# Optimization experiments

Measured on AMD Instinct MI355X. Metric: run time of the kernel, lower is better.

The kernel has to match this reference:

```python
import jax, jax.numpy as jnp
import numpy as np

B, S, D = 4, 4096, 1024
EPS_LN = 1e-5
EPS_REC = 1e-8


def _layernorm(x, g, b):
    mu = jnp.mean(x, axis=-1, keepdims=True)
    var = jnp.mean((x - mu) ** 2, axis=-1, keepdims=True)
    return (x - mu) * jax.lax.rsqrt(var + EPS_LN) * g + b


def setup_inputs() -> dict:
    key = jax.random.key(0)
    ks = jax.random.split(key, 8)
    scale = 1.0 / np.sqrt(D)
    return {
        "x": jax.random.normal(ks[0], (B, S, D), dtype=jnp.float32),
        "x_prev": jax.random.normal(ks[1], (B, S, D), dtype=jnp.float32),
        "mu": jnp.float32(0.5),
        "decay_w": jax.random.uniform(ks[2], (D, 1), jnp.float32, -scale, scale),
        "decay_b": jnp.zeros((1,), jnp.float32),
        "ln1_g": jnp.ones((D,), jnp.float32),
        "ln1_b": jnp.zeros((D,), jnp.float32),
        "Wr_w": jax.random.uniform(ks[3], (D, D), jnp.float32, -scale, scale),
        "Wr_b": jnp.zeros((D,), jnp.float32),
        "Wv_w": jax.random.uniform(ks[4], (D, D), jnp.float32, -scale, scale),
        "Wv_b": jnp.zeros((D,), jnp.float32),
        "ln2_g": jnp.ones((D,), jnp.float32),
        "ln2_b": jnp.zeros((D,), jnp.float32),
    }


def reference(x, x_prev, mu, decay_w, decay_b, ln1_g, ln1_b,
              Wr_w, Wr_b, Wv_w, Wv_b, ln2_g, ln2_b):
    # Shift (token-mix by scalar mu)
    shifted = mu * x + (1.0 - mu) * x_prev  # [B,S,D]

    # SequenceMergingSeq with C = V = W = shifted
    decay = jax.nn.sigmoid(jnp.einsum("bsd,do->bso", shifted, decay_w) + decay_b)  # [B,S,1]
    e = jnp.exp(shifted)                       # [B,S,D]
    ea = jnp.sum(e, axis=-1, keepdims=True)    # [B,S,1]
    ev = e * shifted                           # [B,S,D]

    def step(carry, inp):
        a, b = carry
        d_t, ea_t, ev_t = inp
        a = d_t * a + ea_t            # [B,1]
        b = d_t * b + ev_t            # [B,D]
        return (a, b), b / (a + EPS_REC)

    init = (jnp.zeros((B, 1), shifted.dtype), jnp.zeros((B, D), shifted.dtype))
    xs = (jnp.swapaxes(decay, 0, 1), jnp.swapaxes(ea, 0, 1), jnp.swapaxes(ev, 0, 1))
    _, out_sbd = jax.lax.scan(step, init, xs)  # [S,B,D]
    merged = _layernorm(jnp.swapaxes(out_sbd, 0, 1), ln1_g, ln1_b)  # [B,S,D]

    # StateCoupling
    gate = jax.nn.sigmoid(jnp.einsum("bsd,ed->bse", merged, Wr_w) + Wr_b)
    value = jnp.einsum("bsd,ed->bse", merged, Wv_w) + Wv_b
    coupled = _layernorm(gate * value, ln2_g, ln2_b)

    return shifted + coupled
```

## Files before the change

### kernel.cpp

```cpp
#include <hip/hip_runtime.h>

#define BATCH 4
#define SEQ   4096
#define DIM   1024
#define NCH   512
#define CHK   8
#define NROWS (BATCH*SEQ)

typedef __attribute__((ext_vector_type(4))) float f32x4;
typedef __attribute__((ext_vector_type(8))) short shortx8;
typedef __attribute__((ext_vector_type(4))) short shortx4;

static __device__ __forceinline__ unsigned short f2bf(float f){
    unsigned int u = __float_as_uint(f);
    u += 0x7FFFu + ((u >> 16) & 1u);
    return (unsigned short)(u >> 16);
}
static __device__ __forceinline__ float bf2f(unsigned short h){
    return __uint_as_float(((unsigned int)h) << 16);
}
static __device__ __forceinline__ float sigmoidf_fast(float x){
    return 1.0f / (1.0f + __expf(-x));
}
static __device__ __forceinline__ shortx4 pack4(f32x4 s){
    shortx4 o;
    o.x = (short)f2bf(s.x); o.y = (short)f2bf(s.y);
    o.z = (short)f2bf(s.z); o.w = (short)f2bf(s.w);
    return o;
}

__global__ __launch_bounds__(256) void k_pack_w(
    const float* __restrict__ Wr, const float* __restrict__ Wv,
    unsigned short* __restrict__ Wcat)
{
    const int n = blockIdx.x;
    const int grp = n >> 5, r = n & 31;
    const float* src = (r < 16) ? (Wr + (size_t)(grp*16 + r)*DIM)
                                : (Wv + (size_t)(grp*16 + (r-16))*DIM);
    const int tid = threadIdx.x;
    f32x4 v = reinterpret_cast<const f32x4*>(src)[tid];
    reinterpret_cast<shortx4*>(Wcat)[n*256 + tid] = pack4(v);
}

__global__ __launch_bounds__(256) void k_shift_scan(
    const float* __restrict__ X, const float* __restrict__ XP,
    const float* __restrict__ mu_p, const float* __restrict__ dw,
    const float* __restrict__ db_p,
    unsigned short* __restrict__ shifted,
    float* __restrict__ b_local, float* __restrict__ a_local,
    float* __restrict__ cumP)
{
    const int tid  = threadIdx.x;
    const int lane = tid & 63;
    const int wid  = tid >> 6;
    const int cid  = blockIdx.x*4 + wid;
    const int batch = cid >> 9;
    const int chunk = cid & (NCH-1);
    const int row0  = batch*SEQ + chunk*CHK;

    const float mu = mu_p[0];
    const float om = 1.0f - mu;
    const float db = db_p[0];

    const f32x4* dwv = reinterpret_cast<const f32x4*>(dw);
    const f32x4 w0 = dwv[lane], w1 = dwv[64+lane], w2 = dwv[128+lane], w3 = dwv[192+lane];

    f32x4 b0 = {0,0,0,0}, b1 = {0,0,0,0}, b2 = {0,0,0,0}, b3 = {0,0,0,0};
    float a_run = 0.f, cp = 1.f;

    const f32x4* Xv  = reinterpret_cast<const f32x4*>(X);
    const f32x4* XPv = reinterpret_cast<const f32x4*>(XP);
    f32x4*  BL = reinterpret_cast<f32x4*>(b_local);
    shortx4* SH = reinterpret_cast<shortx4*>(shifted);

    for (int r = 0; r < CHK; ++r){
        const int row = row0 + r;
        const int rb  = row*(DIM/4);

        f32x4 x0 = Xv[rb+lane],     x1 = Xv[rb+64+lane],
              x2 = Xv[rb+128+lane], x3 = Xv[rb+192+lane];
        f32x4 p0 = XPv[rb+lane],     p1 = XPv[rb+64+lane],
              p2 = XPv[rb+128+lane], p3 = XPv[rb+192+lane];
        f32x4 s0 = mu*x0 + om*p0, s1 = mu*x1 + om*p1;
        f32x4 s2 = mu*x2 + om*p2, s3 = mu*x3 + om*p3;

        SH[rb+lane]     = pack4(s0);
        SH[rb+64+lane]  = pack4(s1);
        SH[rb+128+lane] = pack4(s2);
        SH[rb+192+lane] = pack4(s3);

        float dot = s0.x*w0.x + s0.y*w0.y + s0.z*w0.z + s0.w*w0.w
                  + s1.x*w1.x + s1.y*w1.y + s1.z*w1.z + s1.w*w1.w
                  + s2.x*w2.x + s2.y*w2.y + s2.z*w2.z + s2.w*w2.w
                  + s3.x*w3.x + s3.y*w3.y + s3.z*w3.z + s3.w*w3.w;

        f32x4 e0, e1, e2, e3;
        e0.x=__expf(s0.x); e0.y=__expf(s0.y); e0.z=__expf(s0.z); e0.w=__expf(s0.w);
        e1.x=__expf(s1.x); e1.y=__expf(s1.y); e1.z=__expf(s1.z); e1.w=__expf(s1.w);
        e2.x=__expf(s2.x); e2.y=__expf(s2.y); e2.z=__expf(s2.z); e2.w=__expf(s2.w);
        e3.x=__expf(s3.x); e3.y=__expf(s3.y); e3.z=__expf(s3.z); e3.w=__expf(s3.w);
        float ea = e0.x+e0.y+e0.z+e0.w + e1.x+e1.y+e1.z+e1.w
                 + e2.x+e2.y+e2.z+e2.w + e3.x+e3.y+e3.z+e3.w;

        #pragma unroll
        for (int off = 1; off < 64; off <<= 1){
            dot += __shfl_xor(dot, off, 64);
            ea  += __shfl_xor(ea,  off, 64);
        }

        const float dt = sigmoidf_fast(dot + db);
        a_run = dt*a_run + ea;
        cp   *= dt;
        b0 = dt*b0 + e0*s0;  b1 = dt*b1 + e1*s1;
        b2 = dt*b2 + e2*s2;  b3 = dt*b3 + e3*s3;

        BL[rb+lane]     = b0;
        BL[rb+64+lane]  = b1;
        BL[rb+128+lane] = b2;
        BL[rb+192+lane] = b3;
        if (lane == 0){ a_local[row] = a_run; cumP[row] = cp; }
    }
}

__global__ __launch_bounds__(256) void k_combine(
    const float* __restrict__ b_local, const float* __restrict__ a_local,
    const float* __restrict__ cumP,
    float* __restrict__ carryA, float* __restrict__ carryB)
{
    const int batch = blockIdx.x >> 2;
    const int dseg  = blockIdx.x & 3;
    const int d = dseg*256 + threadIdx.x;

    __shared__ float sP[NCH], sA[NCH];
    for (int c = threadIdx.x; c < NCH; c += 256){
        const int er = batch*SEQ + c*CHK + (CHK-1);
        sP[c] = cumP[er];
        sA[c] = a_local[er];
    }
    __syncthreads();

    const float* bl = b_local + (size_t)batch*SEQ*DIM;
    float* cB = carryB + (size_t)batch*NCH*DIM;
    const bool wA = (dseg == 0 && threadIdx.x == 0);

    float cb = 0.f, ca = 0.f;
    float f0 = bl[(0*CHK+CHK-1)*DIM + d];
    float f1 = bl[(1*CHK+CHK-1)*DIM + d];
    float f2 = bl[(2*CHK+CHK-1)*DIM + d];
    float f3 = bl[(3*CHK+CHK-1)*DIM + d];

    for (int c = 0; c < NCH; c += 4){
        const float v0=f0, v1=f1, v2=f2, v3=f3;
        if (c+4 < NCH){
            f0 = bl[((c+4)*CHK+CHK-1)*DIM + d];
            f1 = bl[((c+5)*CHK+CHK-1)*DIM + d];
            f2 = bl[((c+6)*CHK+CHK-1)*DIM + d];
            f3 = bl[((c+7)*CHK+CHK-1)*DIM + d];
        }
        cB[(c+0)*DIM + d] = cb; if (wA) carryA[batch*NCH + c+0] = ca;
        cb = sP[c+0]*cb + v0;   ca = sP[c+0]*ca + sA[c+0];
        cB[(c+1)*DIM + d] = cb; if (wA) carryA[batch*NCH + c+1] = ca;
        cb = sP[c+1]*cb + v1;   ca = sP[c+1]*ca + sA[c+1];
        cB[(c+2)*DIM + d] = cb; if (wA) carryA[batch*NCH + c+2] = ca;
        cb = sP[c+2]*cb + v2;   ca = sP[c+2]*ca + sA[c+2];
        cB[(c+3)*DIM + d] = cb; if (wA) carryA[batch*NCH + c+3] = ca;
        cb = sP[c+3]*cb + v3;   ca = sP[c+3]*ca + sA[c+3];
    }
}

static __device__ __forceinline__ void block_reduce2(float& s, float& s2, float* red, int tid){
    #pragma unroll
    for (int off = 1; off < 64; off <<= 1){
        s  += __shfl_xor(s,  off, 64);
        s2 += __shfl_xor(s2, off, 64);
    }
    const int wid = tid >> 6, lane = tid & 63;
    if (lane == 0){ red[wid] = s; red[4+wid] = s2; }
    __syncthreads();
    s  = red[0]+red[1]+red[2]+red[3];
    s2 = red[4]+red[5]+red[6]+red[7];
}

__global__ __launch_bounds__(256) void k_fix_ln1(
    const float* __restrict__ b_local, const float* __restrict__ a_local,
    const float* __restrict__ cumP, const float* __restrict__ carryA,
    const float* __restrict__ carryB,
    const float* __restrict__ g1, const float* __restrict__ bb1,
    unsigned short* __restrict__ merged)
{
    const int row = blockIdx.x;
    const int batch = row >> 12;
    const int t = row & (SEQ-1);
    const int c = t >> 3;
    const int tid = threadIdx.x;

    const float cpv = cumP[row];
    const float a = a_local[row] + cpv * carryA[batch*NCH + c];
    const float inv_a = 1.0f / (a + 1e-8f);

    f32x4 bl = reinterpret_cast<const f32x4*>(b_local)[row*256 + tid];
    f32x4 cb = reinterpret_cast<const f32x4*>(carryB)[(batch*NCH + c)*256 + tid];
    f32x4 o = (bl + cpv*cb) * inv_a;

    float s  = o.x+o.y+o.z+o.w;
    float s2 = o.x*o.x + o.y*o.y + o.z*o.z + o.w*o.w;
    __shared__ float red[8];
    block_reduce2(s, s2, red, tid);

    const float mean = s * (1.0f/DIM);
    const float rstd = rsqrtf(s2*(1.0f/DIM) - mean*mean + 1e-5f);
    f32x4 gg = reinterpret_cast<const f32x4*>(g1)[tid];
    f32x4 bb = reinterpret_cast<const f32x4*>(bb1)[tid];
    f32x4 m = (o - mean)*rstd*gg + bb;
    reinterpret_cast<shortx4*>(merged)[row*256 + tid] = pack4(m);
}

typedef __attribute__((address_space(3))) unsigned int lds_uint;
typedef __attribute__((address_space(1))) unsigned int glob_uint;
static __device__ __forceinline__ void stage16(const unsigned short* g, unsigned short* l){
    __builtin_amdgcn_global_load_lds((const glob_uint*)g, (lds_uint*)l, 16, 0, 0);
}

__global__ __launch_bounds__(256) void k_gemm(
    const unsigned short* __restrict__ A,
    const unsigned short* __restrict__ Bt,
    const float* __restrict__ rbias, const float* __restrict__ vbias,
    float* __restrict__ gv)
{
    __shared__ __align__(16) unsigned short As[128*32];
    __shared__ __align__(16) unsigned short Bs[128*32];
    const int tid  = threadIdx.x;
    const int lane = tid & 63;
    const int wid  = tid >> 6;
    const int nt = blockIdx.x & 15;
    const int mt = blockIdx.x >> 4;
    const int m0 = mt*128, n0 = nt*128;
    const int wr = wid >> 1, wc = wid & 1;

    f32x4 acc[4][4];
    #pragma unroll
    for (int i = 0; i < 4; ++i)
        #pragma unroll
        for (int j = 0; j < 4; ++j) acc[i][j] = (f32x4){0.f,0.f,0.f,0.f};

    const int srow = tid >> 2;
    const int scol = (tid & 3) << 3;
    const unsigned short* gA0 = A  + (size_t)(m0 + srow)*DIM + scol;
    const unsigned short* gA1 = A  + (size_t)(m0 + 64 + srow)*DIM + scol;
    const unsigned short* gB0 = Bt + (size_t)(n0 + srow)*DIM + scol;
    const unsigned short* gB1 = Bt + (size_t)(n0 + 64 + srow)*DIM + scol;
    unsigned short* lA0 = As + wid*512;
    unsigned short* lA1 = As + 2048 + wid*512;
    unsigned short* lB0 = Bs + wid*512;
    unsigned short* lB1 = Bs + 2048 + wid*512;

    const int fr = lane & 15, fq = lane >> 4;

    for (int kt = 0; kt < DIM/32; ++kt){
        __syncthreads();
        const int ko = kt*32;
        stage16(gA0 + ko, lA0);
        stage16(gA1 + ko, lA1);
        stage16(gB0 + ko, lB0);
        stage16(gB1 + ko, lB1);
        __syncthreads();

        shortx8 af[4], bfv[4];
        #pragma unroll
        for (int f = 0; f < 4; ++f){
            af[f]  = *reinterpret_cast<const shortx8*>(&As[(wr*64 + f*16 + fr)*32 + fq*8]);
            bfv[f] = *reinterpret_cast<const shortx8*>(&Bs[(wc*64 + f*16 + fr)*32 + fq*8]);
        }
        #pragma unroll
        for (int i = 0; i < 4; ++i)
            #pragma unroll
            for (int j = 0; j < 4; ++j)
                acc[i][j] = __builtin_amdgcn_mfma_f32_16x16x32_bf16(af[i], bfv[j], acc[i][j], 0, 0, 0);
    }

    #pragma unroll
    for (int p = 0; p < 2; ++p){
        const int e = (nt*4 + wc*2 + p)*16 + fr;
        const float rbe = rbias[e], vbe = vbias[e];
        #pragma unroll
        for (int i = 0; i < 4; ++i){
            f32x4 ga = acc[i][2*p], va = acc[i][2*p+1];
            const int mrow = m0 + wr*64 + i*16 + fq*4;
            #pragma unroll
            for (int q = 0; q < 4; ++q){
                const float gate = sigmoidf_fast(ga[q] + rbe);
                gv[(size_t)(mrow+q)*DIM + e] = gate * (va[q] + vbe);
            }
        }
    }
}

__global__ __launch_bounds__(256) void k_ln2_res(
    const float* __restrict__ gvb, const unsigned short* __restrict__ shifted,
    const float* __restrict__ g2, const float* __restrict__ b2,
    float* __restrict__ out)
{
    const int row = blockIdx.x, tid = threadIdx.x;
    const int idx = row*256 + tid;
    f32x4 v = reinterpret_cast<const f32x4*>(gvb)[idx];
    float s  = v.x+v.y+v.z+v.w;
    float s2 = v.x*v.x + v.y*v.y + v.z*v.z + v.w*v.w;
    __shared__ float red[8];
    block_reduce2(s, s2, red, tid);
    const float mean = s * (1.0f/DIM);
    const float rstd = rsqrtf(s2*(1.0f/DIM) - mean*mean + 1e-5f);
    f32x4 gg = reinterpret_cast<const f32x4*>(g2)[tid];
    f32x4 bb = reinterpret_cast<const f32x4*>(b2)[tid];
    f32x4 nv = (v - mean)*rstd*gg + bb;
    shortx4 sh = reinterpret_cast<const shortx4*>(shifted)[idx];
    f32x4 o;
    o.x = bf2f((unsigned short)sh.x) + nv.x;
    o.y = bf2f((unsigned short)sh.y) + nv.y;
    o.z = bf2f((unsigned short)sh.z) + nv.z;
    o.w = bf2f((unsigned short)sh.w) + nv.w;
    reinterpret_cast<f32x4*>(out)[idx] = o;
}

extern "C" void kernel_launch(void* const* d_in, const int* in_sizes, int n_in,
                              void* d_out, int out_size, void* d_ws, size_t ws_size,
                              hipStream_t stream)
{
    (void)in_sizes; (void)n_in; (void)out_size; (void)ws_size;
    const float* x     = (const float*)d_in[0];
    const float* xprev = (const float*)d_in[1];
    const float* mu    = (const float*)d_in[2];
    const float* dw    = (const float*)d_in[3];
    const float* db    = (const float*)d_in[4];
    const float* ln1g  = (const float*)d_in[5];
    const float* ln1b  = (const float*)d_in[6];
    const float* Wr    = (const float*)d_in[7];
    const float* Wrb   = (const float*)d_in[8];
    const float* Wv    = (const float*)d_in[9];
    const float* Wvb   = (const float*)d_in[10];
    const float* ln2g  = (const float*)d_in[11];
    const float* ln2b  = (const float*)d_in[12];
    float* out = (float*)d_out;

    char* ws = (char*)d_ws;
    size_t off = 0;
    auto alloc = [&](size_t bytes) -> void* {
        void* p = ws + off;
        off += (bytes + 255) & ~(size_t)255;
        return p;
    };
    unsigned short* shifted = (unsigned short*)alloc((size_t)NROWS*DIM*2);
    float* b_local          = (float*)alloc((size_t)NROWS*DIM*4);
    unsigned short* merged  = (unsigned short*)alloc((size_t)NROWS*DIM*2);
    float* carryB           = (float*)alloc((size_t)BATCH*NCH*DIM*4);
    unsigned short* Wcat    = (unsigned short*)alloc((size_t)2048*1024*2);
    float* a_local          = (float*)alloc((size_t)NROWS*4);
    float* cumP             = (float*)alloc((size_t)NROWS*4);
    float* carryA           = (float*)alloc((size_t)BATCH*NCH*4);
    float* gvbuf = b_local;

    hipLaunchKernelGGL(k_pack_w,    dim3(2048),  dim3(256),  0, stream, Wr, Wv, Wcat);
    hipLaunchKernelGGL(k_shift_scan,dim3(512),   dim3(256),  0, stream,
                       x, xprev, mu, dw, db, shifted, b_local, a_local, cumP);
    hipLaunchKernelGGL(k_combine,   dim3(16),    dim3(256),  0, stream,
                       b_local, a_local, cumP, carryA, carryB);
    hipLaunchKernelGGL(k_fix_ln1,   dim3(16384), dim3(256),  0, stream,
                       b_local, a_local, cumP, carryA, carryB, ln1g, ln1b, merged);
    hipLaunchKernelGGL(k_gemm,      dim3(2048),  dim3(256),  0, stream,
                       merged, Wcat, Wrb, Wvb, gvbuf);
    hipLaunchKernelGGL(k_ln2_res,   dim3(16384), dim3(256),  0, stream,
                       gvbuf, shifted, ln2g, ln2b, out);
}
```

Before: 237.1 us.

## Store scan intermediates in bf16 and pipeline a larger-tile MFMA GEMM

The scan partials (b_local), the chunk carries (carryB) and the gated GEMM output are now stored as bf16 instead of fp32, which halves the main intermediate memory traffic between kernels. The GEMM is rewritten to use 256x128 tiles, 512 threads and a K-step of 64. It triple-buffers LDS through async global-to-LDS loads with explicit waitcnt and barriers, adds a swizzled LDS layout and s_setprio around the MFMA bursts, and writes results out through an LDS-staged, coalesced epilogue. The cost is extra rounding error in the recurrence and the LayerNorm inputs, plus a large LDS footprint (144 KB per block) that limits occupancy.

```diff
diff --git a/kernel.cpp b/kernel.cpp
--- a/kernel.cpp
+++ b/kernel.cpp
@@ -6,6 +6,7 @@
 #define NCH   512
 #define CHK   8
 #define NROWS (BATCH*SEQ)
+#define NT    16
 
 typedef __attribute__((ext_vector_type(4))) float f32x4;
 typedef __attribute__((ext_vector_type(8))) short shortx8;
@@ -26,6 +27,12 @@
     shortx4 o;
     o.x = (short)f2bf(s.x); o.y = (short)f2bf(s.y);
     o.z = (short)f2bf(s.z); o.w = (short)f2bf(s.w);
+    return o;
+}
+static __device__ __forceinline__ f32x4 unpack4(shortx4 s){
+    f32x4 o;
+    o.x = bf2f((unsigned short)s.x); o.y = bf2f((unsigned short)s.y);
+    o.z = bf2f((unsigned short)s.z); o.w = bf2f((unsigned short)s.w);
     return o;
 }
 
@@ -47,7 +54,7 @@
     const float* __restrict__ mu_p, const float* __restrict__ dw,
     const float* __restrict__ db_p,
     unsigned short* __restrict__ shifted,
-    float* __restrict__ b_local, float* __restrict__ a_local,
+    unsigned short* __restrict__ b_local, float* __restrict__ a_local,
     float* __restrict__ cumP)
 {
     const int tid  = threadIdx.x;
@@ -70,7 +77,7 @@
 
     const f32x4* Xv  = reinterpret_cast<const f32x4*>(X);
     const f32x4* XPv = reinterpret_cast<const f32x4*>(XP);
-    f32x4*  BL = reinterpret_cast<f32x4*>(b_local);
+    shortx4* BL = reinterpret_cast<shortx4*>(b_local);
     shortx4* SH = reinterpret_cast<shortx4*>(shifted);
 
     for (int r = 0; r < CHK; ++r){
@@ -114,18 +121,18 @@
         b0 = dt*b0 + e0*s0;  b1 = dt*b1 + e1*s1;
         b2 = dt*b2 + e2*s2;  b3 = dt*b3 + e3*s3;
 
-        BL[rb+lane]     = b0;
-        BL[rb+64+lane]  = b1;
-        BL[rb+128+lane] = b2;
-        BL[rb+192+lane] = b3;
+        BL[rb+lane]     = pack4(b0);
+        BL[rb+64+lane]  = pack4(b1);
+        BL[rb+128+lane] = pack4(b2);
+        BL[rb+192+lane] = pack4(b3);
         if (lane == 0){ a_local[row] = a_run; cumP[row] = cp; }
     }
 }
 
 __global__ __launch_bounds__(256) void k_combine(
-    const float* __restrict__ b_local, const float* __restrict__ a_local,
+    const unsigned short* __restrict__ b_local, const float* __restrict__ a_local,
     const float* __restrict__ cumP,
-    float* __restrict__ carryA, float* __restrict__ carryB)
+    float* __restrict__ carryA, unsigned short* __restrict__ carryB)
 {
     const int batch = blockIdx.x >> 2;
     const int dseg  = blockIdx.x & 3;
@@ -139,31 +146,31 @@
     }
     __syncthreads();
 
-    const float* bl = b_local + (size_t)batch*SEQ*DIM;
-    float* cB = carryB + (size_t)batch*NCH*DIM;
+    const unsigned short* bl = b_local + (size_t)batch*SEQ*DIM;
+    unsigned short* cB = carryB + (size_t)batch*NCH*DIM;
     const bool wA = (dseg == 0 && threadIdx.x == 0);
 
     float cb = 0.f, ca = 0.f;
-    float f0 = bl[(0*CHK+CHK-1)*DIM + d];
-    float f1 = bl[(1*CHK+CHK-1)*DIM + d];
-    float f2 = bl[(2*CHK+CHK-1)*DIM + d];
-    float f3 = bl[(3*CHK+CHK-1)*DIM + d];
+    float f0 = bf2f(bl[(0*CHK+CHK-1)*DIM + d]);
+    float f1 = bf2f(bl[(1*CHK+CHK-1)*DIM + d]);
+    float f2 = bf2f(bl[(2*CHK+CHK-1)*DIM + d]);
+    float f3 = bf2f(bl[(3*CHK+CHK-1)*DIM + d]);
 
     for (int c = 0; c < NCH; c += 4){
         const float v0=f0, v1=f1, v2=f2, v3=f3;
         if (c+4 < NCH){
-            f0 = bl[((c+4)*CHK+CHK-1)*DIM + d];
-            f1 = bl[((c+5)*CHK+CHK-1)*DIM + d];
-            f2 = bl[((c+6)*CHK+CHK-1)*DIM + d];
-            f3 = bl[((c+7)*CHK+CHK-1)*DIM + d];
+            f0 = bf2f(bl[((c+4)*CHK+CHK-1)*DIM + d]);
+            f1 = bf2f(bl[((c+5)*CHK+CHK-1)*DIM + d]);
+            f2 = bf2f(bl[((c+6)*CHK+CHK-1)*DIM + d]);
+            f3 = bf2f(bl[((c+7)*CHK+CHK-1)*DIM + d]);
         }
-        cB[(c+0)*DIM + d] = cb; if (wA) carryA[batch*NCH + c+0] = ca;
+        cB[(c+0)*DIM + d] = f2bf(cb); if (wA) carryA[batch*NCH + c+0] = ca;
         cb = sP[c+0]*cb + v0;   ca = sP[c+0]*ca + sA[c+0];
-        cB[(c+1)*DIM + d] = cb; if (wA) carryA[batch*NCH + c+1] = ca;
+        cB[(c+1)*DIM + d] = f2bf(cb); if (wA) carryA[batch*NCH + c+1] = ca;
         cb = sP[c+1]*cb + v1;   ca = sP[c+1]*ca + sA[c+1];
-        cB[(c+2)*DIM + d] = cb; if (wA) carryA[batch*NCH + c+2] = ca;
+        cB[(c+2)*DIM + d] = f2bf(cb); if (wA) carryA[batch*NCH + c+2] = ca;
         cb = sP[c+2]*cb + v2;   ca = sP[c+2]*ca + sA[c+2];
-        cB[(c+3)*DIM + d] = cb; if (wA) carryA[batch*NCH + c+3] = ca;
+        cB[(c+3)*DIM + d] = f2bf(cb); if (wA) carryA[batch*NCH + c+3] = ca;
         cb = sP[c+3]*cb + v3;   ca = sP[c+3]*ca + sA[c+3];
     }
 }
@@ -182,9 +189,9 @@
 }
 
 __global__ __launch_bounds__(256) void k_fix_ln1(
-    const float* __restrict__ b_local, const float* __restrict__ a_local,
+    const unsigned short* __restrict__ b_local, const float* __restrict__ a_local,
     const float* __restrict__ cumP, const float* __restrict__ carryA,
-    const float* __restrict__ carryB,
+    const unsigned short* __restrict__ carryB,
     const float* __restrict__ g1, const float* __restrict__ bb1,
     unsigned short* __restrict__ merged)
 {
@@ -198,8 +205,8 @@
     const float a = a_local[row] + cpv * carryA[batch*NCH + c];
     const float inv_a = 1.0f / (a + 1e-8f);
 
-    f32x4 bl = reinterpret_cast<const f32x4*>(b_local)[row*256 + tid];
-    f32x4 cb = reinterpret_cast<const f32x4*>(carryB)[(batch*NCH + c)*256 + tid];
+    f32x4 bl = unpack4(reinterpret_cast<const shortx4*>(b_local)[row*256 + tid]);
+    f32x4 cb = unpack4(reinterpret_cast<const shortx4*>(carryB)[(batch*NCH + c)*256 + tid]);
     f32x4 o = (bl + cpv*cb) * inv_a;
 
     float s  = o.x+o.y+o.z+o.w;
@@ -217,92 +224,149 @@
 
 typedef __attribute__((address_space(3))) unsigned int lds_uint;
 typedef __attribute__((address_space(1))) unsigned int glob_uint;
-static __device__ __forceinline__ void stage16(const unsigned short* g, unsigned short* l){
+static __device__ __forceinline__ void gload16(const unsigned short* g, char* l){
     __builtin_amdgcn_global_load_lds((const glob_uint*)g, (lds_uint*)l, 16, 0, 0);
 }
-
-__global__ __launch_bounds__(256) void k_gemm(
+#define SBAR() do { __builtin_amdgcn_sched_barrier(0); __builtin_amdgcn_s_barrier(); __builtin_amdgcn_sched_barrier(0); } while(0)
+
+__global__ __launch_bounds__(512, 2) void k_gemm(
     const unsigned short* __restrict__ A,
     const unsigned short* __restrict__ Bt,
     const float* __restrict__ rbias, const float* __restrict__ vbias,
-    float* __restrict__ gv)
-{
-    __shared__ __align__(16) unsigned short As[128*32];
-    __shared__ __align__(16) unsigned short Bs[128*32];
+    unsigned short* __restrict__ gv)
+{
+    __shared__ __align__(16) char lds[3*49152];
     const int tid  = threadIdx.x;
     const int lane = tid & 63;
     const int wid  = tid >> 6;
-    const int nt = blockIdx.x & 15;
-    const int mt = blockIdx.x >> 4;
-    const int m0 = mt*128, n0 = nt*128;
-    const int wr = wid >> 1, wc = wid & 1;
-
-    f32x4 acc[4][4];
+    const int wm   = wid >> 2;
+    const int wn   = wid & 3;
+
+    const int bid  = blockIdx.x;
+    const int wgid = (bid & 7)*128 + (bid >> 3);
+    const int mt = wgid >> 4, nt = wgid & 15;
+    const int m0 = mt*256, n0 = nt*128;
+
+    const int sr  = lane >> 2;
+    const int scg = (lane & 3) ^ (((lane >> 5) & 1) << 1);
+    const unsigned short* gA = A  + (size_t)(m0 + wid*16 + sr)*DIM + scg*8;
+    const unsigned short* gB = Bt + (size_t)(n0 + wid*16 + sr)*DIM + scg*8;
+
+    const int fr = lane & 15, fq = lane >> 4;
+    const int soff = fr*64 + ((fq*16) ^ ((fr & 8) ? 32 : 0));
+
+    f32x4 acc[8][2];
     #pragma unroll
-    for (int i = 0; i < 4; ++i)
-        #pragma unroll
-        for (int j = 0; j < 4; ++j) acc[i][j] = (f32x4){0.f,0.f,0.f,0.f};
-
-    const int srow = tid >> 2;
-    const int scol = (tid & 3) << 3;
-    const unsigned short* gA0 = A  + (size_t)(m0 + srow)*DIM + scol;
-    const unsigned short* gA1 = A  + (size_t)(m0 + 64 + srow)*DIM + scol;
-    const unsigned short* gB0 = Bt + (size_t)(n0 + srow)*DIM + scol;
-    const unsigned short* gB1 = Bt + (size_t)(n0 + 64 + srow)*DIM + scol;
-    unsigned short* lA0 = As + wid*512;
-    unsigned short* lA1 = As + 2048 + wid*512;
-    unsigned short* lB0 = Bs + wid*512;
-    unsigned short* lB1 = Bs + 2048 + wid*512;
-
-    const int fr = lane & 15, fq = lane >> 4;
-
-    for (int kt = 0; kt < DIM/32; ++kt){
-        __syncthreads();
-        const int ko = kt*32;
-        stage16(gA0 + ko, lA0);
-        stage16(gA1 + ko, lA1);
-        stage16(gB0 + ko, lB0);
-        stage16(gB1 + ko, lB1);
-        __syncthreads();
-
-        shortx8 af[4], bfv[4];
-        #pragma unroll
-        for (int f = 0; f < 4; ++f){
-            af[f]  = *reinterpret_cast<const shortx8*>(&As[(wr*64 + f*16 + fr)*32 + fq*8]);
-            bfv[f] = *reinterpret_cast<const shortx8*>(&Bs[(wc*64 + f*16 + fr)*32 + fq*8]);
+    for (int i = 0; i < 8; ++i){ acc[i][0] = (f32x4){0,0,0,0}; acc[i][1] = (f32x4){0,0,0,0}; }
+
+    auto STAGE_A = [&](int buf, int tk){
+        char* dst = &lds[buf*49152 + wid*2048];
+        const unsigned short* src = gA + tk*64;
+        gload16(src,             dst);
+        gload16(src + 32,        dst + 1024);
+        gload16(src + 128*DIM,      dst + 16384);
+        gload16(src + 128*DIM + 32, dst + 16384 + 1024);
+    };
+    auto STAGE_B = [&](int buf, int tk){
+        char* dst = &lds[buf*49152 + 32768 + wid*2048];
+        const unsigned short* src = gB + tk*64;
+        gload16(src,      dst);
+        gload16(src + 32, dst + 1024);
+    };
+
+    STAGE_A(0, 0); STAGE_B(0, 0);
+    STAGE_A(1, 1); STAGE_B(1, 1);
+    asm volatile("s_waitcnt vmcnt(6)" ::: "memory");
+    SBAR();
+
+    int bc = 0, bn = 2;
+    for (int t = 0; t < NT; ++t){
+        const char* bufA = &lds[bc*49152];
+        const char* bufB = bufA + 32768;
+
+        shortx8 bq[2][2], af[4][2];
+        #pragma unroll
+        for (int nf = 0; nf < 2; ++nf)
+            #pragma unroll
+            for (int ks = 0; ks < 2; ++ks)
+                bq[nf][ks] = *reinterpret_cast<const shortx8*>(bufB + ((wn*2+nf)*2+ks)*1024 + soff);
+        #pragma unroll
+        for (int mf = 0; mf < 4; ++mf)
+            #pragma unroll
+            for (int ks = 0; ks < 2; ++ks)
+                af[mf][ks] = *reinterpret_cast<const shortx8*>(bufA + wm*16384 + (mf*2+ks)*1024 + soff);
+        if (t < NT-2) STAGE_A(bn, t+2);
+        SBAR();
+        __builtin_amdgcn_s_setprio(1);
+        #pragma unroll
+        for (int mf = 0; mf < 4; ++mf)
+            #pragma unroll
+            for (int nf = 0; nf < 2; ++nf){
+                acc[mf][nf] = __builtin_amdgcn_mfma_f32_16x16x32_bf16(af[mf][0], bq[nf][0], acc[mf][nf], 0,0,0);
+                acc[mf][nf] = __builtin_amdgcn_mfma_f32_16x16x32_bf16(af[mf][1], bq[nf][1], acc[mf][nf], 0,0,0);
+            }
+        __builtin_amdgcn_s_setprio(0);
+        SBAR();
+
+        #pragma unroll
+        for (int mf = 0; mf < 4; ++mf)
+            #pragma unroll
+            for (int ks = 0; ks < 2; ++ks)
+                af[mf][ks] = *reinterpret_cast<const shortx8*>(bufA + wm*16384 + ((mf+4)*2+ks)*1024 + soff);
+        if (t < NT-2){
+            STAGE_B(bn, t+2);
+            asm volatile("s_waitcnt vmcnt(6)" ::: "memory");
+        } else {
+            asm volatile("s_waitcnt vmcnt(0)" ::: "memory");
         }
-        #pragma unroll
-        for (int i = 0; i < 4; ++i)
+        SBAR();
+        __builtin_amdgcn_s_setprio(1);
+        #pragma unroll
+        for (int mf = 0; mf < 4; ++mf)
             #pragma unroll
-            for (int j = 0; j < 4; ++j)
-                acc[i][j] = __builtin_amdgcn_mfma_f32_16x16x32_bf16(af[i], bfv[j], acc[i][j], 0, 0, 0);
-    }
-
+            for (int nf = 0; nf < 2; ++nf){
+                acc[mf+4][nf] = __builtin_amdgcn_mfma_f32_16x16x32_bf16(af[mf][0], bq[nf][0], acc[mf+4][nf], 0,0,0);
+                acc[mf+4][nf] = __builtin_amdgcn_mfma_f32_16x16x32_bf16(af[mf][1], bq[nf][1], acc[mf+4][nf], 0,0,0);
+            }
+        __builtin_amdgcn_s_setprio(0);
+        SBAR();
+
+        bc = (bc == 2) ? 0 : bc+1;
+        bn = (bn == 2) ? 0 : bn+1;
+    }
+
+    __syncthreads();
+    unsigned short* ep = reinterpret_cast<unsigned short*>(lds);
+    const int e = (nt*4 + wn)*16 + fr;
+    const float rbe = rbias[e], vbe = vbias[e];
     #pragma unroll
-    for (int p = 0; p < 2; ++p){
-        const int e = (nt*4 + wc*2 + p)*16 + fr;
-        const float rbe = rbias[e], vbe = vbias[e];
-        #pragma unroll
-        for (int i = 0; i < 4; ++i){
-            f32x4 ga = acc[i][2*p], va = acc[i][2*p+1];
-            const int mrow = m0 + wr*64 + i*16 + fq*4;
-            #pragma unroll
-            for (int q = 0; q < 4; ++q){
-                const float gate = sigmoidf_fast(ga[q] + rbe);
-                gv[(size_t)(mrow+q)*DIM + e] = gate * (va[q] + vbe);
-            }
+    for (int mf = 0; mf < 8; ++mf){
+        const int rbase = wm*128 + mf*16 + fq*4;
+        #pragma unroll
+        for (int q = 0; q < 4; ++q){
+            const float g = sigmoidf_fast(acc[mf][0][q] + rbe);
+            const float v = acc[mf][1][q] + vbe;
+            ep[(rbase + q)*64 + wn*16 + fr] = f2bf(g*v);
         }
     }
+    __syncthreads();
+    #pragma unroll
+    for (int p = 0; p < 4; ++p){
+        const int row = p*64 + (tid >> 3);
+        const int cg8 = tid & 7;
+        shortx8 val = *reinterpret_cast<const shortx8*>(&ep[row*64 + cg8*8]);
+        *reinterpret_cast<shortx8*>(&gv[(size_t)(m0+row)*DIM + nt*64 + cg8*8]) = val;
+    }
 }
 
 __global__ __launch_bounds__(256) void k_ln2_res(
-    const float* __restrict__ gvb, const unsigned short* __restrict__ shifted,
+    const unsigned short* __restrict__ gvb, const unsigned short* __restrict__ shifted,
     const float* __restrict__ g2, const float* __restrict__ b2,
     float* __restrict__ out)
 {
     const int row = blockIdx.x, tid = threadIdx.x;
     const int idx = row*256 + tid;
-    f32x4 v = reinterpret_cast<const f32x4*>(gvb)[idx];
+    f32x4 v = unpack4(reinterpret_cast<const shortx4*>(gvb)[idx]);
     float s  = v.x+v.y+v.z+v.w;
     float s2 = v.x*v.x + v.y*v.y + v.z*v.z + v.w*v.w;
     __shared__ float red[8];
@@ -312,13 +376,8 @@
     f32x4 gg = reinterpret_cast<const f32x4*>(g2)[tid];
     f32x4 bb = reinterpret_cast<const f32x4*>(b2)[tid];
     f32x4 nv = (v - mean)*rstd*gg + bb;
-    shortx4 sh = reinterpret_cast<const shortx4*>(shifted)[idx];
-    f32x4 o;
-    o.x = bf2f((unsigned short)sh.x) + nv.x;
-    o.y = bf2f((unsigned short)sh.y) + nv.y;
-    o.z = bf2f((unsigned short)sh.z) + nv.z;
-    o.w = bf2f((unsigned short)sh.w) + nv.w;
-    reinterpret_cast<f32x4*>(out)[idx] = o;
+    f32x4 sh = unpack4(reinterpret_cast<const shortx4*>(shifted)[idx]);
+    reinterpret_cast<f32x4*>(out)[idx] = sh + nv;
 }
 
 extern "C" void kernel_launch(void* const* d_in, const int* in_sizes, int n_in,
@@ -349,24 +408,24 @@
         return p;
     };
     unsigned short* shifted = (unsigned short*)alloc((size_t)NROWS*DIM*2);
-    float* b_local          = (float*)alloc((size_t)NROWS*DIM*4);
+    unsigned short* b_local = (unsigned short*)alloc((size_t)NROWS*DIM*2);
     unsigned short* merged  = (unsigned short*)alloc((size_t)NROWS*DIM*2);
-    float* carryB           = (float*)alloc((size_t)BATCH*NCH*DIM*4);
+    unsigned short* carryB  = (unsigned short*)alloc((size_t)BATCH*NCH*DIM*2);
     unsigned short* Wcat    = (unsigned short*)alloc((size_t)2048*1024*2);
     float* a_local          = (float*)alloc((size_t)NROWS*4);
     float* cumP             = (float*)alloc((size_t)NROWS*4);
     float* carryA           = (float*)alloc((size_t)BATCH*NCH*4);
-    float* gvbuf = b_local;
-
-    hipLaunchKernelGGL(k_pack_w,    dim3(2048),  dim3(256),  0, stream, Wr, Wv, Wcat);
-    hipLaunchKernelGGL(k_shift_scan,dim3(512),   dim3(256),  0, stream,
+    unsigned short* gvbuf   = b_local;
+
+    hipLaunchKernelGGL(k_pack_w,    dim3(2048),  dim3(256), 0, stream, Wr, Wv, Wcat);
+    hipLaunchKernelGGL(k_shift_scan,dim3(512),   dim3(256), 0, stream,
                        x, xprev, mu, dw, db, shifted, b_local, a_local, cumP);
-    hipLaunchKernelGGL(k_combine,   dim3(16),    dim3(256),  0, stream,
+    hipLaunchKernelGGL(k_combine,   dim3(16),    dim3(256), 0, stream,
                        b_local, a_local, cumP, carryA, carryB);
-    hipLaunchKernelGGL(k_fix_ln1,   dim3(16384), dim3(256),  0, stream,
+    hipLaunchKernelGGL(k_fix_ln1,   dim3(16384), dim3(256), 0, stream,
                        b_local, a_local, cumP, carryA, carryB, ln1g, ln1b, merged);
-    hipLaunchKernelGGL(k_gemm,      dim3(2048),  dim3(256),  0, stream,
+    hipLaunchKernelGGL(k_gemm,      dim3(1024),  dim3(512), 0, stream,
                        merged, Wcat, Wrb, Wvb, gvbuf);
-    hipLaunchKernelGGL(k_ln2_res,   dim3(16384), dim3(256),  0, stream,
+    hipLaunchKernelGGL(k_ln2_res,   dim3(16384), dim3(256), 0, stream,
                        gvbuf, shifted, ln2g, ln2b, out);
 }
```

Result: no change. 236.9 us (-0.1%).
